# Optimization experiments

Measured on AMD Instinct MI355X. Metric: run time of the kernel, lower is better.

Reference implementation:

```python
import jax, jax.numpy as jnp
import numpy as np

N = 4608      # total nodes (48 graphs x 96 nodes)
B = 48
NPG = 96
D = 512       # vec_dim
XD = 16       # x_dim
E = N * 32    # GAT edges
L = 6         # GAT layers


def _w(k, shape, fan_in):
    return jax.random.normal(k, shape, jnp.float32) * (1.0 / np.sqrt(fan_in))


def setup_inputs() -> dict:
    key = jax.random.key(0)
    ks = jax.random.split(key, 24)
    x = jax.random.normal(ks[0], (N, XD), jnp.float32)
    xyz = jax.random.normal(ks[1], (N, 3), jnp.float32)
    edge_index = jax.random.randint(ks[2], (2, E), 0, N, dtype=jnp.int32)
    ptr = (jnp.arange(B + 1) * NPG).astype(jnp.int32)
    # complete graph with replacement per segment (torch.combinations order: i<=j)
    i, j = np.triu_indices(NPG)
    offs = (np.arange(B) * NPG)[:, None]
    cloud_edge_index = jnp.asarray(
        np.stack([(i[None, :] + offs).reshape(-1), (j[None, :] + offs).reshape(-1)]),
        jnp.int32)
    return {
        'x': x, 'edge_index': edge_index, 'ptr': ptr, 'xyz': xyz,
        'cloud_edge_index': cloud_edge_index,
        'x_proj_w': _w(ks[3], (XD, D), XD), 'x_proj_b': jnp.zeros((D,), jnp.float32),
        'gat_wl': _w(ks[4], (L, D, D), D), 'gat_bl': jnp.zeros((L, D), jnp.float32),
        'gat_wr': _w(ks[5], (L, D, D), D), 'gat_br': jnp.zeros((L, D), jnp.float32),
        'gat_att': _w(ks[6], (L, D), D), 'gat_bias': jnp.zeros((L, D), jnp.float32),
        'gat_ln_g': jnp.ones((L - 1, D), jnp.float32), 'gat_ln_b': jnp.zeros((L - 1, D), jnp.float32),
        'cg_xyz_w': _w(ks[7], (3, D), 3),
        'cg_bn_g': jnp.ones((D,), jnp.float32), 'cg_bn_b': jnp.zeros((D,), jnp.float32),
        'cg_lin1_w': _w(ks[8], (D, D), D), 'cg_lin1_b': jnp.zeros((D,), jnp.float32),
        'cg_ln_g': jnp.ones((D,), jnp.float32), 'cg_ln_b': jnp.zeros((D,), jnp.float32),
        'lin_w': _w(ks[9], (D, D), D), 'lin_b': jnp.zeros((D,), jnp.float32),
        'bn_g': jnp.ones((D,), jnp.float32), 'bn_b': jnp.zeros((D,), jnp.float32),
    }


def _batchnorm(t, g, b):
    mu = t.mean(0)
    v = ((t - mu) ** 2).mean(0)
    return (t - mu) / jnp.sqrt(v + 1e-5) * g + b


def _forward(x, edge_index, cloud_edge_index, x_proj_w, x_proj_b, gat_wl, gat_bl,
             gat_wr, gat_br, gat_att, gat_bias, gat_ln_g, gat_ln_b, cg_xyz_w,
             cg_bn_g, cg_bn_b, cg_lin1_w, cg_lin1_b, cg_ln_g, cg_ln_b,
             lin_w, lin_b, bn_g, bn_b, xyz):
    n = x.shape[0]
    h = x @ x_proj_w + x_proj_b  # [N, D]
    # ---- GATv2 stack (heads=1, self-loops added, eval mode: no dropout) ----
    loops = jnp.arange(n, dtype=edge_index.dtype)
    ei = jnp.concatenate([edge_index, jnp.stack([loops, loops])], axis=1)
    src, dst = ei[0], ei[1]
    xg = h
    for l in range(L):
        xl = xg @ gat_wl[l] + gat_bl[l]
        xr = xg @ gat_wr[l] + gat_br[l]
        e = jax.nn.leaky_relu(xl[src] + xr[dst], 0.2) @ gat_att[l]  # [E+N]
        m = jax.ops.segment_max(e, dst, num_segments=n)
        ew = jnp.exp(e - m[dst])
        den = jax.ops.segment_sum(ew, dst, num_segments=n)
        alpha = ew / den[dst]
        out = jax.ops.segment_sum(alpha[:, None] * xl[src], dst, num_segments=n) + gat_bias[l]
        if l < L - 1:
            # PyG LayerNorm, mode='graph', batch=None: normalize over all elements
            mu = out.mean()
            sd = jnp.sqrt(((out - mu) ** 2).mean())
            out = (out - mu) / (sd + 1e-5) * gat_ln_g[l] + gat_ln_b[l]
            out = jax.nn.relu(out)
        xg = out
    # ---- CloudGraph (complete graph gather-compute-scatter) ----
    a, b = cloud_edge_index[0], cloud_edge_index[1]
    rx = h[a] - h[b]          # [Ec, D]
    rz = xyz[a] - xyz[b]      # [Ec, 3]
    sq = (rz ** 2).sum(-1)
    dist = jnp.where(sq > 0, jnp.sqrt(jnp.where(sq > 0, sq, 1.0)), 0.0)
    w = jnp.exp(-dist)[:, None]
    p1 = jax.ops.segment_sum(jax.nn.relu((w * rx) @ cg_lin1_w + cg_lin1_b), a, num_segments=n)
    mu1 = p1.mean(-1, keepdims=True)
    v1 = ((p1 - mu1) ** 2).mean(-1, keepdims=True)
    ln1 = (p1 - mu1) / jnp.sqrt(v1 + 1e-5) * cg_ln_g + cg_ln_b
    p2 = jax.ops.segment_sum(jax.nn.relu(rz @ cg_xyz_w), a, num_segments=n)
    xc = h + ln1 + _batchnorm(p2, cg_bn_g, cg_bn_b)
    # ---- fuse + final norm ----
    return _batchnorm((h + xg + xc) @ lin_w + lin_b, bn_g, bn_b)


def reference(x, edge_index, ptr, xyz, cloud_edge_index, x_proj_w, x_proj_b,
              gat_wl, gat_bl, gat_wr, gat_br, gat_att, gat_bias, gat_ln_g,
              gat_ln_b, cg_xyz_w, cg_bn_g, cg_bn_b, cg_lin1_w, cg_lin1_b,
              cg_ln_g, cg_ln_b, lin_w, lin_b, bn_g, bn_b):
    return _forward(x, edge_index, cloud_edge_index, x_proj_w, x_proj_b, gat_wl,
                    gat_bl, gat_wr, gat_br, gat_att, gat_bias, gat_ln_g,
                    gat_ln_b, cg_xyz_w, cg_bn_g, cg_bn_b, cg_lin1_w, cg_lin1_b,
                    cg_ln_g, cg_ln_b, lin_w, lin_b, bn_g, bn_b, xyz)
```

## Files before the change

kernel.cpp:

```cpp
#include <hip/hip_runtime.h>
#include <hip/hip_bf16.h>

#define NN 4608
#define BG 48
#define NPG 96
#define DD 512
#define XDIM 16
#define EREAL 147456
#define NLAYER 6
#define NK 262144
#define TRIU 4656

typedef __hip_bfloat16 bf16;
typedef short short8 __attribute__((ext_vector_type(8)));
typedef short shortx4 __attribute__((ext_vector_type(4)));
typedef float f32x4 __attribute__((ext_vector_type(4)));
typedef float f32x2 __attribute__((ext_vector_type(2)));

__device__ __forceinline__ float s2f(short s) {
  return __uint_as_float(((unsigned int)(unsigned short)s) << 16);
}
__device__ __forceinline__ short f2bs(float f) {
  bf16 h = __float2bfloat16(f);
  short s;
  __builtin_memcpy(&s, &h, 2);
  return s;
}
__device__ __forceinline__ void f8x4(unsigned int w, float* o) {
  f32x2 a = __builtin_amdgcn_cvt_pk_f32_fp8(w, false);
  f32x2 b = __builtin_amdgcn_cvt_pk_f32_fp8(w, true);
  o[0] = a[0]; o[1] = a[1]; o[2] = b[0]; o[3] = b[1];
}

typedef const __attribute__((address_space(1))) unsigned int ga_u32;
typedef __attribute__((address_space(3))) unsigned int ls_u32;
__device__ __forceinline__ void gl16(const void* g, void* l) {
  __builtin_amdgcn_global_load_lds((ga_u32*)g, (ls_u32*)l, 16, 0, 0);
}

__global__ __launch_bounds__(256) void k_wt(const float* __restrict__ wl,
                                            const float* __restrict__ wr,
                                            const float* __restrict__ cg,
                                            const float* __restrict__ lin,
                                            bf16* __restrict__ Wt,
                                            int* __restrict__ counts,
                                            float* __restrict__ statsAll) {
  if (blockIdx.z == 0) {
    int id = (blockIdx.y * 16 + blockIdx.x) * 256 + threadIdx.x;
    if (id < NN) counts[id] = 0;
    if (id < 5 * 32) statsAll[id] = 0.f;
  }
  __shared__ float tile[32][33];
  int z = blockIdx.z;
  const float* src = (z < 6) ? wl + (size_t)z * NK
                   : (z < 12) ? wr + (size_t)(z - 6) * NK
                   : (z == 12) ? cg : lin;
  bf16* dst = Wt + (size_t)z * NK;
  int c = threadIdx.x & 31;
  int r0 = threadIdx.x >> 5;
  int bx = blockIdx.x * 32, by = blockIdx.y * 32;
#pragma unroll
  for (int i = 0; i < 4; i++) {
    int r = r0 + i * 8;
    tile[r][c] = src[(size_t)(by + r) * 512 + bx + c];
  }
  __syncthreads();
#pragma unroll
  for (int i = 0; i < 4; i++) {
    int r = r0 + i * 8;
    dst[(size_t)(bx + r) * 512 + by + c] = __float2bfloat16(tile[c][r]);
  }
}

__global__ void k_xproj(const float* __restrict__ x, const float* __restrict__ w,
                        const float* __restrict__ b, const int* __restrict__ ei,
                        const float* __restrict__ xyz,
                        bf16* __restrict__ h_bf, int* __restrict__ counts,
                        float* __restrict__ ep) {
  int i = blockIdx.x * blockDim.x + threadIdx.x;
  if (i >= NN * DD) return;
  if (i < EREAL) atomicAdd(&counts[ei[EREAL + i]], 1);
  if (i < NN * NPG) {
    int n = i / NPG, e = i - n * NPG;
    int p = n % NPG;
    if (e < NPG - p) {
      int g = n / NPG;
      int slot = g * TRIU + p * NPG - (p * (p - 1)) / 2 + e;
      int j = n + e;
      float dx = xyz[n * 3] - xyz[j * 3];
      float dy = xyz[n * 3 + 1] - xyz[j * 3 + 1];
      float dz = xyz[n * 3 + 2] - xyz[j * 3 + 2];
      float sq = dx * dx + dy * dy + dz * dz;
      float dist = (sq > 0.f) ? sqrtf(sq) : 0.f;
      float4 v;
      v.x = dx; v.y = dy; v.z = dz; v.w = __expf(-dist);
      *(float4*)&ep[(size_t)slot * 4] = v;
    }
  }
  int n = i >> 9, d = i & 511;
  float acc = b[d];
#pragma unroll
  for (int k = 0; k < XDIM; k++) acc += x[n * XDIM + k] * w[k * DD + d];
  h_bf[i] = __float2bfloat16(acc);
}

__global__ void k_scan(const int* __restrict__ counts, int* offsets, int* cursor) {
  __shared__ int part[256];
  int t = threadIdx.x;
  int base = t * 18;
  int s = 0;
#pragma unroll
  for (int i = 0; i < 18; i++) s += counts[base + i];
  part[t] = s;
  __syncthreads();
  for (int off = 1; off < 256; off <<= 1) {
    int v = part[t];
    int u = (t >= off) ? part[t - off] : 0;
    __syncthreads();
    part[t] = v + u;
    __syncthreads();
  }
  int run = t ? part[t - 1] : 0;
#pragma unroll
  for (int i = 0; i < 18; i++) {
    offsets[base + i] = run;
    cursor[base + i] = run;
    run += counts[base + i];
  }
  if (t == 0) offsets[NN] = EREAL;
}

__global__ __launch_bounds__(256) void k_ln(bf16* __restrict__ xg,
                                            const float* __restrict__ stats,
                                            const float* __restrict__ g,
                                            const float* __restrict__ b,
                                            const float* __restrict__ p2a,
                                            const float* __restrict__ p2b,
                                            float* __restrict__ colsum,
                                            float* __restrict__ colsq) {
  if ((int)blockIdx.x >= 1152) {
    int r0 = (blockIdx.x - 1152) * 32;
    int c0 = threadIdx.x;
    float s0 = 0.f, q0 = 0.f, s1 = 0.f, q1 = 0.f;
    for (int r = r0; r < r0 + 32; ++r) {
      float v = p2a[(size_t)r * 512 + c0] + p2b[(size_t)r * 512 + c0];
      s0 += v; q0 += v * v;
      float w = p2a[(size_t)r * 512 + c0 + 256] + p2b[(size_t)r * 512 + c0 + 256];
      s1 += w; q1 += w * w;
    }
    atomicAdd(&colsum[c0], s0);
    atomicAdd(&colsq[c0], q0);
    atomicAdd(&colsum[c0 + 256], s1);
    atomicAdd(&colsq[c0 + 256], q1);
    return;
  }
  float s = 0.f, ss = 0.f;
#pragma unroll
  for (int i = 0; i < 16; i++) { s += stats[i]; ss += stats[16 + i]; }
  const float invM = 1.f / ((float)NN * (float)DD);
  float mu = s * invM;
  float var = ss * invM - mu * mu;
  float sd = sqrtf(fmaxf(var, 0.f));
  float inv = 1.f / (sd + 1e-5f);
  int i = blockIdx.x * 256 + threadIdx.x;
  int base = i * 8;
  int d0 = base & 511;
  short8 raw = *(const short8*)&xg[base];
  short8 pk;
#pragma unroll
  for (int k = 0; k < 8; k++) {
    float t = fmaxf((s2f(raw[k]) - mu) * inv * g[d0 + k] + b[d0 + k], 0.f);
    pk[k] = f2bs(t);
  }
  *(short8*)&xg[base] = pk;
}

__device__ __forceinline__ void gemm_tile(
    const bf16* __restrict__ Abf, const bf16* __restrict__ B,
    const float* __restrict__ bias,
    float* __restrict__ C, bf16* __restrict__ Cb, unsigned char* __restrict__ Cf8,
    float* __restrict__ csum, float* __restrict__ csq,
    int m0, int n0, bf16* As, bf16* Bs, float* cs, float* cq) {
  int tid = threadIdx.x;
  int lane = tid & 63, wid = tid >> 6;
  int mh = (wid >> 1) * 64, nh = (wid & 1) * 32;
  int l15 = lane & 15, quad = lane >> 4;
  int lr8 = lane >> 3, ls8 = lane & 7;
  int c16l = ls8 ^ lr8;
  int swzr = (l15 & 7) * 8;

  if (csum && tid < 64) { cs[tid] = 0.f; cq[tid] = 0.f; }

  const bf16* aSrc = Abf + (size_t)(m0 + wid * 32 + lr8) * 512 + c16l * 8;
  const bf16* bSrc = B   + (size_t)(n0 + wid * 16 + lr8) * 512 + c16l * 8;

#define STAGE(bi, kt) do {                                                   \
    gl16(aSrc + (kt) * 64,            As + (bi) * 8192 + (wid * 32     ) * 64); \
    gl16(aSrc + (kt) * 64 +  8 * 512, As + (bi) * 8192 + (wid * 32 +  8) * 64); \
    gl16(aSrc + (kt) * 64 + 16 * 512, As + (bi) * 8192 + (wid * 32 + 16) * 64); \
    gl16(aSrc + (kt) * 64 + 24 * 512, As + (bi) * 8192 + (wid * 32 + 24) * 64); \
    gl16(bSrc + (kt) * 64,            Bs + (bi) * 4096 + (wid * 16     ) * 64); \
    gl16(bSrc + (kt) * 64 +  8 * 512, Bs + (bi) * 4096 + (wid * 16 +  8) * 64); \
  } while (0)

  f32x4 acc[4][2];
#pragma unroll
  for (int mt = 0; mt < 4; mt++)
#pragma unroll
    for (int nt = 0; nt < 2; nt++) acc[mt][nt] = (f32x4)0.f;

  STAGE(0, 0);
  __syncthreads();

#pragma unroll
  for (int kt = 0; kt < 8; kt++) {
    const int cur = kt & 1;
    if (kt < 7) STAGE(cur ^ 1, kt + 1);
    short8 af[2][4], bfr[2][2];
#pragma unroll
    for (int kk = 0; kk < 2; kk++) {
#pragma unroll
      for (int mt = 0; mt < 4; mt++)
        af[kk][mt] = *(const short8*)&As[cur * 8192 + (mh + mt * 16 + l15) * 64 +
                                        (((kk * 4 + quad) * 8) ^ swzr)];
#pragma unroll
      for (int nt = 0; nt < 2; nt++)
        bfr[kk][nt] = *(const short8*)&Bs[cur * 4096 + (nh + nt * 16 + l15) * 64 +
                                         (((kk * 4 + quad) * 8) ^ swzr)];
    }
#pragma unroll
    for (int kk = 0; kk < 2; kk++)
#pragma unroll
      for (int mt = 0; mt < 4; mt++)
#pragma unroll
        for (int nt = 0; nt < 2; nt++)
          acc[mt][nt] = __builtin_amdgcn_mfma_f32_16x16x32_bf16(
              bfr[kk][nt], af[kk][mt], acc[mt][nt], 0, 0, 0);
    __syncthreads();
  }
#undef STAGE

  float colS[2][4] = {{0.f,0.f,0.f,0.f},{0.f,0.f,0.f,0.f}};
  float colQ[2][4] = {{0.f,0.f,0.f,0.f},{0.f,0.f,0.f,0.f}};
  float bv[2][4] = {{0.f,0.f,0.f,0.f},{0.f,0.f,0.f,0.f}};
#pragma unroll
  for (int nt = 0; nt < 2; nt++) {
    if (bias) {
      float4 b4 = *(const float4*)&bias[n0 + nh + nt * 16 + quad * 4];
      bv[nt][0] = b4.x; bv[nt][1] = b4.y; bv[nt][2] = b4.z; bv[nt][3] = b4.w;
    }
  }
#pragma unroll
  for (int mt = 0; mt < 4; mt++) {
    int row = m0 + mh + mt * 16 + l15;
#pragma unroll
    for (int nt = 0; nt < 2; nt++) {
      int col0 = n0 + nh + nt * 16 + quad * 4;
      float v[4];
#pragma unroll
      for (int r2 = 0; r2 < 4; r2++) {
        v[r2] = acc[mt][nt][r2] + bv[nt][r2];
        if (csum) { colS[nt][r2] += v[r2]; colQ[nt][r2] += v[r2] * v[r2]; }
      }
      if (C) {
        float4 o; o.x = v[0]; o.y = v[1]; o.z = v[2]; o.w = v[3];
        *(float4*)&C[(size_t)row * 512 + col0] = o;
      }
      if (Cb) {
        shortx4 o;
#pragma unroll
        for (int r2 = 0; r2 < 4; r2++) o[r2] = f2bs(v[r2]);
        *(shortx4*)&Cb[(size_t)row * 512 + col0] = o;
      }
      if (Cf8) {
        unsigned int u = __builtin_amdgcn_cvt_pk_fp8_f32(v[0], v[1], 0, false);
        u = __builtin_amdgcn_cvt_pk_fp8_f32(v[2], v[3], u, true);
        *(unsigned int*)&Cf8[(size_t)row * 512 + col0] = u;
      }
    }
  }
  if (csum) {
#pragma unroll
    for (int nt = 0; nt < 2; nt++)
#pragma unroll
      for (int r2 = 0; r2 < 4; r2++) {
        atomicAdd(&cs[nh + nt * 16 + quad * 4 + r2], colS[nt][r2]);
        atomicAdd(&cq[nh + nt * 16 + quad * 4 + r2], colQ[nt][r2]);
      }
    __syncthreads();
    if (tid < 64) {
      atomicAdd(&csum[n0 + tid], cs[tid]);
      atomicAdd(&csq[n0 + tid], cq[tid]);
    }
  }
}

__global__ __launch_bounds__(256) void k_gemm(
    const bf16* __restrict__ Abf,
    const bf16* __restrict__ B0, const bf16* __restrict__ B1,
    const float* __restrict__ bias0, const float* __restrict__ bias1,
    float* __restrict__ C0,
    bf16* __restrict__ Cb0, bf16* __restrict__ Cb1,
    unsigned char* __restrict__ Cf8_0,
    float* __restrict__ csum, float* __restrict__ csq, int nzl) {
  __shared__ __align__(16) bf16 As[2 * 128 * 64];
  __shared__ __align__(16) bf16 Bs[2 * 64 * 64];
  __shared__ float cs[64], cq[64];
  int cpx = gridDim.x >> 3;
  int wgid = (blockIdx.x & 7) * cpx + (blockIdx.x >> 3);
  int mi = wgid >> nzl;
  int r = wgid & ((1 << nzl) - 1);
  int z = r >> 3;
  int m0 = mi * 128, n0 = (r & 7) * 64;
  gemm_tile(Abf, z ? B1 : B0, z ? bias1 : bias0,
            z ? nullptr : C0, z ? Cb1 : Cb0, z ? nullptr : Cf8_0,
            csum, csq, m0, n0, As, Bs, cs, cq);
}

__global__ __launch_bounds__(256) void k_gemm_l0(
    const bf16* __restrict__ h_bf,
    const bf16* __restrict__ Bl, const bf16* __restrict__ Br,
    const float* __restrict__ biasl, const float* __restrict__ biasr,
    bf16* __restrict__ xr_bf, unsigned char* __restrict__ xl_f8,
    const bf16* __restrict__ Bg1, float* __restrict__ g1f,
    float* __restrict__ zptr,
    const int* __restrict__ ei, int* __restrict__ cursor, int* __restrict__ ssrc) {
  __shared__ __align__(16) bf16 As[2 * 128 * 64];
  __shared__ __align__(16) bf16 Bs[2 * 64 * 64];
  int b = blockIdx.x;
  if (b < 576) {
    int cpx = 576 >> 3;
    int wgid = (b & 7) * cpx + (b >> 3);
    int mi = wgid >> 4;
    int r = wgid & 15;
    int z = r >> 3;
    int m0 = mi * 128, n0 = (r & 7) * 64;
    gemm_tile(h_bf, z ? Br : Bl, z ? biasr : biasl,
              nullptr, z ? xr_bf : nullptr, z ? nullptr : xl_f8,
              nullptr, nullptr, m0, n0, As, Bs, nullptr, nullptr);
  } else if (b < 864) {
    int b2 = b - 576;
    if (b2 == 0) {
      for (int i = threadIdx.x; i < 1024; i += 256) zptr[i] = 0.f;
    }
    int cpx = 288 >> 3;
    int wgid = (b2 & 7) * cpx + (b2 >> 3);
    int mi = wgid >> 3;
    int r = wgid & 7;
    int m0 = mi * 128, n0 = r * 64;
    gemm_tile(h_bf, Bg1, nullptr, g1f, nullptr, nullptr,
              nullptr, nullptr, m0, n0, As, Bs, nullptr, nullptr);
  } else {
    int e = (b - 864) * 256 + threadIdx.x;
    int s = ei[e], d = ei[EREAL + e];
    int pos = atomicAdd(&cursor[d], 1);
    ssrc[pos] = s;
  }
}

__device__ __forceinline__ void edge_block(
    const unsigned char* __restrict__ xl8, const bf16* __restrict__ xr,
    const float* __restrict__ att, const float* __restrict__ bias,
    const int* __restrict__ offs, const int* __restrict__ ssrc,
    bf16* __restrict__ out, float* __restrict__ statsOut,
    float* redS, float* redSS,
    const float* __restrict__ p1a, const float* __restrict__ p1b,
    const float* __restrict__ p2a, const float* __restrict__ p2b,
    const bf16* __restrict__ h_bf,
    const float* __restrict__ colsum, const float* __restrict__ colsq,
    const float* __restrict__ lng, const float* __restrict__ lnb,
    const float* __restrict__ bng, const float* __restrict__ bnb,
    bf16* __restrict__ s_bf, float* __restrict__ zptr) {
  if (zptr && blockIdx.x == 0) {
    for (int i = threadIdx.x; i < 1024; i += 256) zptr[i] = 0.f;
  }
  int wave = (blockIdx.x * blockDim.x + threadIdx.x) >> 6;
  int lane = threadIdx.x & 63;
  int wid = threadIdx.x >> 6;
  if (wave < NN) {
    int n = wave;
    int base = lane * 8;
    float xrv[8], attv[8], acc[8];
    short8 xr8 = *(const short8*)&xr[(size_t)n * 512 + base];
#pragma unroll
    for (int k = 0; k < 8; k++) {
      xrv[k] = s2f(xr8[k]);
      attv[k] = att[base + k];
    }
    float m0, lsum;
    {
      uint2 q = *(const uint2*)&xl8[(size_t)n * 512 + base];
      float xs[8];
      f8x4(q.x, xs);
      f8x4(q.y, xs + 4);
      float sc0 = 0.f;
#pragma unroll
      for (int k = 0; k < 8; k++) {
        acc[k] = xs[k];
        float t = xs[k] + xrv[k];
        t = (t > 0.f) ? t : 0.2f * t;
        sc0 += attv[k] * t;
      }
#pragma unroll
      for (int off = 32; off >= 1; off >>= 1) sc0 += __shfl_xor(sc0, off, 64);
      m0 = sc0;
      lsum = 1.f;
    }
    int e0 = offs[n], e1 = offs[n + 1];
    int e = e0;
    for (; e + 3 < e1; e += 4) {
      int s0 = ssrc[e], s1 = ssrc[e + 1], s2 = ssrc[e + 2], s3 = ssrc[e + 3];
      uint2 q0 = *(const uint2*)&xl8[(size_t)s0 * 512 + base];
      uint2 q1 = *(const uint2*)&xl8[(size_t)s1 * 512 + base];
      uint2 q2 = *(const uint2*)&xl8[(size_t)s2 * 512 + base];
      uint2 q3 = *(const uint2*)&xl8[(size_t)s3 * 512 + base];
      float x0[8], x1[8], x2[8], x3[8];
      f8x4(q0.x, x0); f8x4(q0.y, x0 + 4);
      f8x4(q1.x, x1); f8x4(q1.y, x1 + 4);
      f8x4(q2.x, x2); f8x4(q2.y, x2 + 4);
      f8x4(q3.x, x3); f8x4(q3.y, x3 + 4);
      float c0 = 0.f, c1 = 0.f, c2 = 0.f, c3 = 0.f;
#pragma unroll
      for (int k = 0; k < 8; k++) {
        float t0 = x0[k] + xrv[k]; t0 = (t0 > 0.f) ? t0 : 0.2f * t0; c0 += attv[k] * t0;
        float t1 = x1[k] + xrv[k]; t1 = (t1 > 0.f) ? t1 : 0.2f * t1; c1 += attv[k] * t1;
        float t2 = x2[k] + xrv[k]; t2 = (t2 > 0.f) ? t2 : 0.2f * t2; c2 += attv[k] * t2;
        float t3 = x3[k] + xrv[k]; t3 = (t3 > 0.f) ? t3 : 0.2f * t3; c3 += attv[k] * t3;
      }
#pragma unroll
      for (int off = 32; off >= 1; off >>= 1) {
        c0 += __shfl_xor(c0, off, 64);
        c1 += __shfl_xor(c1, off, 64);
        c2 += __shfl_xor(c2, off, 64);
        c3 += __shfl_xor(c3, off, 64);
      }
      float p0 = __expf(c0 - m0), pp1 = __expf(c1 - m0);
      float pp2 = __expf(c2 - m0), p3 = __expf(c3 - m0);
      lsum += p0 + pp1 + pp2 + p3;
#pragma unroll
      for (int k = 0; k < 8; k++)
        acc[k] += p0 * x0[k] + pp1 * x1[k] + pp2 * x2[k] + p3 * x3[k];
    }
    for (; e < e1; ++e) {
      int s0 = ssrc[e];
      uint2 q = *(const uint2*)&xl8[(size_t)s0 * 512 + base];
      float x0[8];
      f8x4(q.x, x0);
      f8x4(q.y, x0 + 4);
      float sc0 = 0.f;
#pragma unroll
      for (int k = 0; k < 8; k++) {
        float t0 = x0[k] + xrv[k];
        t0 = (t0 > 0.f) ? t0 : 0.2f * t0;
        sc0 += attv[k] * t0;
      }
#pragma unroll
      for (int off = 32; off >= 1; off >>= 1) sc0 += __shfl_xor(sc0, off, 64);
      float p0 = __expf(sc0 - m0);
      lsum += p0;
#pragma unroll
      for (int k = 0; k < 8; k++) acc[k] += p0 * x0[k];
    }
    float inv = 1.f / lsum;
    float o[8];
    float s = 0.f, ss = 0.f;
    short8 o8;
#pragma unroll
    for (int k = 0; k < 8; k++) {
      o[k] = acc[k] * inv + bias[base + k];
      s += o[k];
      ss += o[k] * o[k];
      o8[k] = f2bs(o[k]);
    }
    *(short8*)&out[(size_t)n * 512 + base] = o8;
    if (statsOut) {
#pragma unroll
      for (int off = 32; off >= 1; off >>= 1) {
        s += __shfl_xor(s, off, 64);
        ss += __shfl_xor(ss, off, 64);
      }
      if (lane == 0) { redS[wid] = s; redSS[wid] = ss; }
    }
    if (s_bf) {
      size_t rb = (size_t)n * 512 + base;
      float v[8];
      float sp = 0.f;
#pragma unroll
      for (int k = 0; k < 8; k++) {
        v[k] = p1a[rb + k] + p1b[rb + k];
        sp += v[k];
      }
#pragma unroll
      for (int off = 32; off >= 1; off >>= 1) sp += __shfl_xor(sp, off, 64);
      float mu = sp * (1.f / 512.f);
      float ssp = 0.f;
#pragma unroll
      for (int k = 0; k < 8; k++) {
        float t = v[k] - mu;
        ssp += t * t;
      }
#pragma unroll
      for (int off = 32; off >= 1; off >>= 1) ssp += __shfl_xor(ssp, off, 64);
      float linv = 1.f / sqrtf(ssp * (1.f / 512.f) + 1e-5f);
      short8 hb = *(const short8*)&h_bf[rb];
      short8 e8;
#pragma unroll
      for (int k = 0; k < 8; k++) {
        int d = base + k;
        float ln1 = (v[k] - mu) * linv * lng[d] + lnb[d];
        float cmu = colsum[d] * (1.f / NN);
        float cvar = colsq[d] * (1.f / NN) - cmu * cmu;
        float cinv = 1.f / sqrtf(fmaxf(cvar, 0.f) + 1e-5f);
        float p2v = p2a[rb + k] + p2b[rb + k];
        float bnv = (p2v - cmu) * cinv * bng[d] + bnb[d];
        float outv = 2.f * s2f(hb[k]) + s2f(o8[k]) + ln1 + bnv;
        e8[k] = f2bs(outv);
      }
      *(short8*)&s_bf[rb] = e8;
    }
  }
  if (statsOut) {
    __syncthreads();
    if (threadIdx.x == 0) {
      float a = redS[0] + redS[1] + redS[2] + redS[3];
      float b = redSS[0] + redSS[1] + redSS[2] + redSS[3];
      int slot = blockIdx.x & 15;
      atomicAdd(&statsOut[slot], a);
      atomicAdd(&statsOut[16 + slot], b);
    }
  }
}

__device__ __forceinline__ void cloud_wave(
    const float* __restrict__ g1f, const float* __restrict__ ep,
    const float* __restrict__ lin1b, const float* __restrict__ w3,
    float* __restrict__ p1c, float* __restrict__ p2c, int w, int lane) {
  int qh = w & 1;
  int c = (w >> 1) & 1;
  int pi = w >> 2;
  int g = pi / 48, pp = pi % 48;
  int d0 = qh * 256 + lane * 4;
  float4 bb4 = *(const float4*)&lin1b[d0];
  float4 w04 = *(const float4*)&w3[d0];
  float4 w14 = *(const float4*)&w3[512 + d0];
  float4 w24 = *(const float4*)&w3[1024 + d0];
  float bb[4] = {bb4.x, bb4.y, bb4.z, bb4.w};
  float w0[4] = {w04.x, w04.y, w04.z, w04.w};
  float w1[4] = {w14.x, w14.y, w14.z, w14.w};
  float w2[4] = {w24.x, w24.y, w24.z, w24.w};

#pragma unroll
  for (int half = 0; half < 2; half++) {
    int p = half ? (NPG - 1 - pp) : pp;
    int n = g * NPG + p;
    int cnt = NPG - p;
    int h = cnt >> 1;
    int eBeg = c ? h : 0;
    int eEnd = c ? cnt : h;
    int slot0 = g * TRIU + p * NPG - (p * (p - 1)) / 2;
    const float* grow = &g1f[(size_t)n * 512 + d0];
    float4 g4 = *(const float4*)grow;
    float gi[4] = {g4.x, g4.y, g4.z, g4.w};
    float a1[4] = {0.f,0.f,0.f,0.f}, a2[4] = {0.f,0.f,0.f,0.f};
    float b1[4] = {0.f,0.f,0.f,0.f}, b2[4] = {0.f,0.f,0.f,0.f};
    int e = eBeg;
    for (; e + 3 < eEnd; e += 4) {
      int sb = __builtin_amdgcn_readfirstlane(slot0 + e);
      float4 pa = *(const float4*)&ep[(size_t)sb * 4];
      float4 pb = *(const float4*)&ep[(size_t)(sb + 1) * 4];
      float4 pc = *(const float4*)&ep[(size_t)(sb + 2) * 4];
      float4 pd = *(const float4*)&ep[(size_t)(sb + 3) * 4];
      float4 xa = *(const float4*)&grow[(size_t)e * 512];
      float4 xb = *(const float4*)&grow[(size_t)(e + 1) * 512];
      float4 xc = *(const float4*)&grow[(size_t)(e + 2) * 512];
      float4 xd = *(const float4*)&grow[(size_t)(e + 3) * 512];
      float xaf[4] = {xa.x, xa.y, xa.z, xa.w};
      float xbf[4] = {xb.x, xb.y, xb.z, xb.w};
      float xcf[4] = {xc.x, xc.y, xc.z, xc.w};
      float xdf[4] = {xd.x, xd.y, xd.z, xd.w};
      float t;
#pragma unroll
      for (int k = 0; k < 4; k++) {
        t = fmaf(pa.w, gi[k] - xaf[k], bb[k]); a1[k] += fmaxf(t, 0.f);
        t = fmaf(pb.w, gi[k] - xbf[k], bb[k]); b1[k] += fmaxf(t, 0.f);
        t = fmaf(pc.w, gi[k] - xcf[k], bb[k]); a1[k] += fmaxf(t, 0.f);
        t = fmaf(pd.w, gi[k] - xdf[k], bb[k]); b1[k] += fmaxf(t, 0.f);
        t = pa.x * w0[k] + pa.y * w1[k] + pa.z * w2[k]; a2[k] += fmaxf(t, 0.f);
        t = pb.x * w0[k] + pb.y * w1[k] + pb.z * w2[k]; b2[k] += fmaxf(t, 0.f);
        t = pc.x * w0[k] + pc.y * w1[k] + pc.z * w2[k]; a2[k] += fmaxf(t, 0.f);
        t = pd.x * w0[k] + pd.y * w1[k] + pd.z * w2[k]; b2[k] += fmaxf(t, 0.f);
      }
    }
    for (; e < eEnd; ++e) {
      float4 pa = *(const float4*)&ep[(size_t)(slot0 + e) * 4];
      float4 xa = *(const float4*)&grow[(size_t)e * 512];
      float xaf[4] = {xa.x, xa.y, xa.z, xa.w};
      float t;
#pragma unroll
      for (int k = 0; k < 4; k++) {
        t = fmaf(pa.w, gi[k] - xaf[k], bb[k]); a1[k] += fmaxf(t, 0.f);
        t = pa.x * w0[k] + pa.y * w1[k] + pa.z * w2[k]; a2[k] += fmaxf(t, 0.f);
      }
    }
    float4 o1, o2;
    o1.x = a1[0] + b1[0]; o1.y = a1[1] + b1[1];
    o1.z = a1[2] + b1[2]; o1.w = a1[3] + b1[3];
    o2.x = a2[0] + b2[0]; o2.y = a2[1] + b2[1];
    o2.z = a2[2] + b2[2]; o2.w = a2[3] + b2[3];
    *(float4*)&p1c[(size_t)n * 512 + d0] = o1;
    *(float4*)&p2c[(size_t)n * 512 + d0] = o2;
  }
}

__global__ __launch_bounds__(256) void k_gat_edge(
    const unsigned char* __restrict__ xl8, const bf16* __restrict__ xr,
    const float* __restrict__ att, const float* __restrict__ bias,
    const int* __restrict__ offs, const int* __restrict__ ssrc,
    bf16* __restrict__ out, float* __restrict__ statsOut,
    const float* __restrict__ p1a, const float* __restrict__ p1b,
    const float* __restrict__ p2a, const float* __restrict__ p2b,
    const bf16* __restrict__ h_bf,
    const float* __restrict__ colsum, const float* __restrict__ colsq,
    const float* __restrict__ lng, const float* __restrict__ lnb,
    const float* __restrict__ bng, const float* __restrict__ bnb,
    bf16* __restrict__ s_bf, float* __restrict__ zptr) {
  __shared__ float redS[4], redSS[4];
  edge_block(xl8, xr, att, bias, offs, ssrc, out, statsOut, redS, redSS,
             p1a, p1b, p2a, p2b, h_bf, colsum, colsq, lng, lnb, bng, bnb,
             s_bf, zptr);
}

__global__ __launch_bounds__(256) void k_edge_cloud(
    const unsigned char* __restrict__ xl8, const bf16* __restrict__ xr,
    const float* __restrict__ att, const float* __restrict__ bias,
    const int* __restrict__ offs, const int* __restrict__ ssrc,
    bf16* __restrict__ out, float* __restrict__ statsOut,
    const float* __restrict__ g1f, const float* __restrict__ ep,
    const float* __restrict__ lin1b, const float* __restrict__ w3,
    float* __restrict__ p1a, float* __restrict__ p1b,
    float* __restrict__ p2a, float* __restrict__ p2b) {
  __shared__ float redS[4], redSS[4];
  if ((int)blockIdx.x < 1152) {
    edge_block(xl8, xr, att, bias, offs, ssrc, out, statsOut, redS, redSS,
               nullptr, nullptr, nullptr, nullptr, nullptr, nullptr, nullptr,
               nullptr, nullptr, nullptr, nullptr, nullptr, nullptr);
  } else {
    int w = (blockIdx.x - 1152) * 4 + (threadIdx.x >> 6);
    int c = (w >> 1) & 1;
    cloud_wave(g1f, ep, lin1b, w3, c ? p1b : p1a, c ? p2b : p2a,
               w, threadIdx.x & 63);
  }
}

__global__ void k_bn_out(const float* __restrict__ y, const float* __restrict__ colsum,
                         const float* __restrict__ colsq, const float* __restrict__ g,
                         const float* __restrict__ b, float* __restrict__ out) {
  int i = blockIdx.x * blockDim.x + threadIdx.x;
  if (i >= NN * DD) return;
  int d = i & 511;
  float mu = colsum[d] * (1.f / NN);
  float var = colsq[d] * (1.f / NN) - mu * mu;
  float inv = 1.f / sqrtf(fmaxf(var, 0.f) + 1e-5f);
  out[i] = (y[i] - mu) * inv * g[d] + b[d];
}

extern "C" void kernel_launch(void* const* d_in, const int* in_sizes, int n_in,
                              void* d_out, int out_size, void* d_ws, size_t ws_size,
                              hipStream_t stream) {
  const float* x = (const float*)d_in[0];
  const int* ei = (const int*)d_in[1];
  const float* xyz = (const float*)d_in[3];
  const float* x_proj_w = (const float*)d_in[5];
  const float* x_proj_b = (const float*)d_in[6];
  const float* gat_wl = (const float*)d_in[7];
  const float* gat_bl = (const float*)d_in[8];
  const float* gat_wr = (const float*)d_in[9];
  const float* gat_br = (const float*)d_in[10];
  const float* gat_att = (const float*)d_in[11];
  const float* gat_bias = (const float*)d_in[12];
  const float* gat_ln_g = (const float*)d_in[13];
  const float* gat_ln_b = (const float*)d_in[14];
  const float* cg_xyz_w = (const float*)d_in[15];
  const float* cg_bn_g = (const float*)d_in[16];
  const float* cg_bn_b = (const float*)d_in[17];
  const float* cg_lin1_w = (const float*)d_in[18];
  const float* cg_lin1_b = (const float*)d_in[19];
  const float* cg_ln_g = (const float*)d_in[20];
  const float* cg_ln_b = (const float*)d_in[21];
  const float* lin_w = (const float*)d_in[22];
  const float* lin_b = (const float*)d_in[23];
  const float* bn_g = (const float*)d_in[24];
  const float* bn_b = (const float*)d_in[25];

  const size_t ND = (size_t)NN * DD;
  char* w = (char*)d_ws;
  float* p1a = (float*)w;      w += ND * 4;
  float* p2a = (float*)w;      w += ND * 4;
  float* p1b = (float*)w;      w += ND * 4;
  float* p2b = (float*)w;      w += ND * 4;
  float* g1f = (float*)w;      w += ND * 4;
  bf16* h_bf = (bf16*)w;       w += ND * 2;
  bf16* xg_bf = (bf16*)w;      w += ND * 2;
  bf16* xr_bf = (bf16*)w;      w += ND * 2;
  unsigned char* xl_f8 = (unsigned char*)w; w += ND;
  bf16* Wt = (bf16*)w;         w += (size_t)14 * NK * 2;
  float* eparam = (float*)w;   w += (size_t)BG * TRIU * 16;
  int* counts = (int*)w;       w += NN * 4;
  int* offs = (int*)w;         w += (NN + 4) * 4;
  int* cursor = (int*)w;       w += NN * 4;
  int* ssrc = (int*)w;         w += EREAL * 4;
  float* statsAll = (float*)w; w += 5 * 32 * 4;
  float* colsum = (float*)w;   w += 512 * 4;
  float* colsq = (float*)w;    w += 512 * 4;
  float* colsum2 = (float*)w;  w += 512 * 4;
  float* colsq2 = (float*)w;   w += 512 * 4;
  float* y = p1a;
  bf16* s_bf = h_bf;

  const int TPB = 256;
  const int ND_BLK = (int)((ND + TPB - 1) / TPB);

  k_wt<<<dim3(16, 16, 14), TPB, 0, stream>>>(gat_wl, gat_wr, cg_lin1_w, lin_w, Wt,
                                             counts, statsAll);
  k_xproj<<<ND_BLK, TPB, 0, stream>>>(x, x_proj_w, x_proj_b, ei, xyz, h_bf,
                                      counts, eparam);
  k_scan<<<1, 256, 0, stream>>>(counts, offs, cursor);

  k_gemm_l0<<<1440, TPB, 0, stream>>>(h_bf, Wt, Wt + (size_t)6 * NK,
                                      gat_bl, gat_br, xr_bf, xl_f8,
                                      Wt + (size_t)12 * NK, g1f, colsum,
                                      ei, cursor, ssrc);
  k_edge_cloud<<<1152 + 2304, TPB, 0, stream>>>(
      xl_f8, xr_bf, gat_att, gat_bias, offs, ssrc, xg_bf, statsAll,
      g1f, eparam, cg_lin1_b, cg_xyz_w, p1a, p1b, p2a, p2b);

  for (int l = 1; l < NLAYER; l++) {
    k_ln<<<(l == 1) ? 1296 : 1152, TPB, 0, stream>>>(
        xg_bf, statsAll + 32 * (l - 1),
        gat_ln_g + (size_t)(l - 1) * DD, gat_ln_b + (size_t)(l - 1) * DD,
        (l == 1) ? p2a : nullptr, (l == 1) ? p2b : nullptr, colsum, colsq);
    k_gemm<<<576, TPB, 0, stream>>>(
        xg_bf, Wt + (size_t)l * NK, Wt + (size_t)(6 + l) * NK,
        gat_bl + l * DD, gat_br + l * DD, nullptr, nullptr, xr_bf,
        xl_f8, nullptr, nullptr, 4);
    float* sOut = (l < NLAYER - 1) ? statsAll + 32 * l : nullptr;
    bool last = (l == NLAYER - 1);
    k_gat_edge<<<NN / 4, TPB, 0, stream>>>(
        xl_f8, xr_bf, gat_att + l * DD, gat_bias + l * DD, offs, ssrc,
        xg_bf, sOut,
        last ? p1a : nullptr, last ? p1b : nullptr,
        last ? p2a : nullptr, last ? p2b : nullptr,
        last ? h_bf : nullptr,
        last ? colsum : nullptr, last ? colsq : nullptr,
        last ? cg_ln_g : nullptr, last ? cg_ln_b : nullptr,
        last ? cg_bn_g : nullptr, last ? cg_bn_b : nullptr,
        last ? s_bf : nullptr, last ? colsum2 : nullptr);
  }

  k_gemm<<<288, TPB, 0, stream>>>(
      s_bf, Wt + (size_t)13 * NK, Wt + (size_t)13 * NK, lin_b, lin_b,
      y, nullptr, nullptr, nullptr, colsum2, colsq2, 3);
  k_bn_out<<<ND_BLK, TPB, 0, stream>>>(y, colsum2, colsq2, bn_g, bn_b,
                                       (float*)d_out);
}
```

Measured before the change: 511.9 us.

## Spread cloud-branch work across the first four GAT edge kernels

Drops the separate combined edge+cloud launch and merges the two kernels into one. The 2304 cloud blocks are split into four chunks of 576, each appended to the GAT edge kernel launch of layers 0–3 through a chunk offset. The cloud BatchNorm statistics pass moves from the layer-1 LayerNorm launch to the layer-5 one, after all chunks are done. The aim is to overlap the cloud work with the latency-bound edge aggregation in several layers rather than making one layer much longer. In exchange, each edge kernel now carries extra arguments and a block-index branch.

```diff
diff --git a/kernel.cpp b/kernel.cpp
--- a/kernel.cpp
+++ b/kernel.cpp
@@ -623,31 +623,20 @@
     const float* __restrict__ colsum, const float* __restrict__ colsq,
     const float* __restrict__ lng, const float* __restrict__ lnb,
     const float* __restrict__ bng, const float* __restrict__ bnb,
-    bf16* __restrict__ s_bf, float* __restrict__ zptr) {
-  __shared__ float redS[4], redSS[4];
-  edge_block(xl8, xr, att, bias, offs, ssrc, out, statsOut, redS, redSS,
-             p1a, p1b, p2a, p2b, h_bf, colsum, colsq, lng, lnb, bng, bnb,
-             s_bf, zptr);
-}
-
-__global__ __launch_bounds__(256) void k_edge_cloud(
-    const unsigned char* __restrict__ xl8, const bf16* __restrict__ xr,
-    const float* __restrict__ att, const float* __restrict__ bias,
-    const int* __restrict__ offs, const int* __restrict__ ssrc,
-    bf16* __restrict__ out, float* __restrict__ statsOut,
+    bf16* __restrict__ s_bf, float* __restrict__ zptr,
     const float* __restrict__ g1f, const float* __restrict__ ep,
-    const float* __restrict__ lin1b, const float* __restrict__ w3,
-    float* __restrict__ p1a, float* __restrict__ p1b,
-    float* __restrict__ p2a, float* __restrict__ p2b) {
+    const float* __restrict__ lin1b_c, const float* __restrict__ w3,
+    float* __restrict__ cp1a, float* __restrict__ cp1b,
+    float* __restrict__ cp2a, float* __restrict__ cp2b, int chunkStart) {
   __shared__ float redS[4], redSS[4];
   if ((int)blockIdx.x < 1152) {
     edge_block(xl8, xr, att, bias, offs, ssrc, out, statsOut, redS, redSS,
-               nullptr, nullptr, nullptr, nullptr, nullptr, nullptr, nullptr,
-               nullptr, nullptr, nullptr, nullptr, nullptr, nullptr);
+               p1a, p1b, p2a, p2b, h_bf, colsum, colsq, lng, lnb, bng, bnb,
+               s_bf, zptr);
   } else {
-    int w = (blockIdx.x - 1152) * 4 + (threadIdx.x >> 6);
+    int w = ((int)blockIdx.x - 1152 + chunkStart) * 4 + (threadIdx.x >> 6);
     int c = (w >> 1) & 1;
-    cloud_wave(g1f, ep, lin1b, w3, c ? p1b : p1a, c ? p2b : p2a,
+    cloud_wave(g1f, ep, lin1b_c, w3, c ? cp1b : cp1a, c ? cp2b : cp2a,
                w, threadIdx.x & 63);
   }
 }
@@ -730,22 +719,22 @@
                                       gat_bl, gat_br, xr_bf, xl_f8,
                                       Wt + (size_t)12 * NK, g1f, colsum,
                                       ei, cursor, ssrc);
-  k_edge_cloud<<<1152 + 2304, TPB, 0, stream>>>(
-      xl_f8, xr_bf, gat_att, gat_bias, offs, ssrc, xg_bf, statsAll,
-      g1f, eparam, cg_lin1_b, cg_xyz_w, p1a, p1b, p2a, p2b);
-
-  for (int l = 1; l < NLAYER; l++) {
-    k_ln<<<(l == 1) ? 1296 : 1152, TPB, 0, stream>>>(
-        xg_bf, statsAll + 32 * (l - 1),
-        gat_ln_g + (size_t)(l - 1) * DD, gat_ln_b + (size_t)(l - 1) * DD,
-        (l == 1) ? p2a : nullptr, (l == 1) ? p2b : nullptr, colsum, colsq);
-    k_gemm<<<576, TPB, 0, stream>>>(
-        xg_bf, Wt + (size_t)l * NK, Wt + (size_t)(6 + l) * NK,
-        gat_bl + l * DD, gat_br + l * DD, nullptr, nullptr, xr_bf,
-        xl_f8, nullptr, nullptr, 4);
+
+  for (int l = 0; l < NLAYER; l++) {
+    if (l > 0) {
+      k_ln<<<(l == 5) ? 1296 : 1152, TPB, 0, stream>>>(
+          xg_bf, statsAll + 32 * (l - 1),
+          gat_ln_g + (size_t)(l - 1) * DD, gat_ln_b + (size_t)(l - 1) * DD,
+          p2a, p2b, colsum, colsq);
+      k_gemm<<<576, TPB, 0, stream>>>(
+          xg_bf, Wt + (size_t)l * NK, Wt + (size_t)(6 + l) * NK,
+          gat_bl + l * DD, gat_br + l * DD, nullptr, nullptr, xr_bf,
+          xl_f8, nullptr, nullptr, 4);
+    }
     float* sOut = (l < NLAYER - 1) ? statsAll + 32 * l : nullptr;
     bool last = (l == NLAYER - 1);
-    k_gat_edge<<<NN / 4, TPB, 0, stream>>>(
+    bool hasCloud = (l < 4);
+    k_gat_edge<<<1152 + (hasCloud ? 576 : 0), TPB, 0, stream>>>(
         xl_f8, xr_bf, gat_att + l * DD, gat_bias + l * DD, offs, ssrc,
         xg_bf, sOut,
         last ? p1a : nullptr, last ? p1b : nullptr,
@@ -754,7 +743,9 @@
         last ? colsum : nullptr, last ? colsq : nullptr,
         last ? cg_ln_g : nullptr, last ? cg_ln_b : nullptr,
         last ? cg_bn_g : nullptr, last ? cg_bn_b : nullptr,
-        last ? s_bf : nullptr, last ? colsum2 : nullptr);
+        last ? s_bf : nullptr, last ? colsum2 : nullptr,
+        hasCloud ? g1f : nullptr, eparam, cg_lin1_b, cg_xyz_w,
+        p1a, p1b, p2a, p2b, l * 576);
   }
 
   k_gemm<<<288, TPB, 0, stream>>>(
```

New measurement: 496.8 us, median of 3. 1.03x faster.
